# Performance work log

Hardware: AMD Instinct MI355X
Metric: run time of the kernel (lower is better)

The kernel has to match this reference:

```python
import jax, jax.numpy as jnp
import numpy as np

N_NODES = 50000
N_EDGES = 800000
N_GRAPHS = 64
D = 96              # input_dim = hidden_dim = output_dim
N_GIN = 4           # num_layers - 1 GINConv layers
N_HEADS = 5         # num_layers linear_prediction heads
BN_EPS = 1e-5


def setup_inputs() -> dict:
    key = jax.random.key(0)
    ks = jax.random.split(key, 16)
    s = 1.0 / np.sqrt(D)
    h = jax.random.normal(ks[0], (N_NODES, D), dtype=jnp.float32)
    src = jax.random.randint(ks[1], (N_EDGES,), 0, N_NODES, dtype=jnp.int32)
    dst = jax.random.randint(ks[2], (N_EDGES,), 0, N_NODES, dtype=jnp.int32)
    # sorted node->graph ids; deterministic so every graph is non-empty
    graph_ids = (jnp.arange(N_NODES, dtype=jnp.int32) * N_GRAPHS) // N_NODES
    return {
        "h": h,
        # GIN layer MLPs (num_mlp_layers=2): Linear -> BN -> ReLU -> Linear
        "gin_W1": jax.random.uniform(ks[3], (N_GIN, D, D), jnp.float32, -s, s),
        "gin_b1": jax.random.uniform(ks[4], (N_GIN, D), jnp.float32, -s, s),
        "gin_bn1_g": jnp.ones((N_GIN, D), jnp.float32),
        "gin_bn1_b": jnp.zeros((N_GIN, D), jnp.float32),
        "gin_W2": jax.random.uniform(ks[5], (N_GIN, D, D), jnp.float32, -s, s),
        "gin_b2": jax.random.uniform(ks[6], (N_GIN, D), jnp.float32, -s, s),
        # per-layer outer BatchNorm1d
        "bn_g": jnp.ones((N_GIN, D), jnp.float32),
        "bn_b": jnp.zeros((N_GIN, D), jnp.float32),
        # shared PReLU parameter (nn.PReLU default: 1 param, init 0.25)
        "prelu_a": jnp.full((1,), 0.25, jnp.float32),
        # linear_prediction heads
        "lin_W": jax.random.uniform(ks[7], (N_HEADS, D, D), jnp.float32, -s, s),
        "lin_b": jax.random.uniform(ks[8], (N_HEADS, D), jnp.float32, -s, s),
        "src": src,
        "dst": dst,
        "graph_ids": graph_ids,
    }


def _batchnorm(x, gamma, beta):
    # training-mode batch statistics over the node dim (biased variance, as torch)
    m = jnp.mean(x, axis=0)
    v = jnp.var(x, axis=0)
    return gamma * (x - m) * jax.lax.rsqrt(v + BN_EPS) + beta


def reference(h, gin_W1, gin_b1, gin_bn1_g, gin_bn1_b, gin_W2, gin_b2,
              bn_g, bn_b, prelu_a, lin_W, lin_b, src, dst, graph_ids):
    hidden_rep = [h]
    for l in range(N_GIN):
        # GINConv, sum aggregation, eps=0 (learn_eps=False): (1+eps)*h + sum_{j in N(i)} h_j
        agg = jax.ops.segment_sum(h[src], dst, num_segments=N_NODES)  # [N, D]
        z = h + agg
        # apply_func MLP: Linear -> BN -> ReLU -> Linear
        z = jax.nn.relu(_batchnorm(z @ gin_W1[l] + gin_b1[l], gin_bn1_g[l], gin_bn1_b[l]))
        z = z @ gin_W2[l] + gin_b2[l]
        # outer BatchNorm + PReLU
        z = _batchnorm(z, bn_g[l], bn_b[l])
        h = jnp.where(z >= 0, z, prelu_a * z)
        hidden_rep.append(h)
    # max graph pooling + per-layer linear heads (dropout = identity in eval)
    reps = []
    for l, hr in enumerate(hidden_rep):
        pooled = jax.ops.segment_max(hr, graph_ids, num_segments=N_GRAPHS)  # [B, D]
        reps.append(pooled @ lin_W[l] + lin_b[l])
    # layer_aggregation='cat': stack on dim=-1 then flatten -> [B, D * (N_GIN+1)]
    return jnp.stack(reps, axis=-1).reshape(N_GRAPHS, -1)
```

## Files before the change

kernel.cpp:

```cpp
#include <hip/hip_runtime.h>
#include <hip/hip_bf16.h>

#define N_NODES 50000
#define N_EDGES 800000
#define N_GRAPHS 64
#define D 96
#define N_GIN 4
#define BN_EPS 1e-5f
#define PCH 64
#define GEMM_GRID 782
#define LP 104
#define ELLCAP 64
#define SENT 50000

#define P1_BLOCKS 256
#define EPB 3125
#define BSH 8
#define BNODES 256
#define NBUCK 196
#define SPITCH 33

typedef __bf16 bf16;
typedef __bf16 bf16x8 __attribute__((ext_vector_type(8)));
typedef float f32x4 __attribute__((ext_vector_type(4)));
typedef unsigned short u16;
typedef unsigned int u32;
typedef unsigned short u16x8 __attribute__((ext_vector_type(8)));

__device__ inline unsigned enc(float f) {
    unsigned b = __float_as_uint(f);
    return (b & 0x80000000u) ? ~b : (b | 0x80000000u);
}
__device__ inline float dec(unsigned u) {
    return __uint_as_float((u & 0x80000000u) ? (u ^ 0x80000000u) : ~u);
}

__global__ void k_prolog(const float* __restrict__ h, bf16* __restrict__ hb,
                         bf16* __restrict__ hb1,
                         const float* __restrict__ W1, const float* __restrict__ W2,
                         bf16* __restrict__ wf, float* __restrict__ stats,
                         unsigned* __restrict__ pooledu) {
    int b = blockIdx.x;
    int tid = threadIdx.x;
    if (b < 2344) {
        int e = (b * 256 + tid) * 8;
        if (e >= N_NODES * D) return;
        float4 v0 = *(const float4*)(h + e);
        float4 v1 = *(const float4*)(h + e + 4);
        bf16x8 o;
        o[0] = (bf16)v0.x; o[1] = (bf16)v0.y; o[2] = (bf16)v0.z; o[3] = (bf16)v0.w;
        o[4] = (bf16)v1.x; o[5] = (bf16)v1.y; o[6] = (bf16)v1.z; o[7] = (bf16)v1.w;
        *(bf16x8*)(hb + e) = o;
    } else if (b < 2352) {
        int mat = b - 2344;
        const float* src = (mat < 4) ? (W1 + mat * D * D) : (W2 + (mat - 4) * D * D);
        bf16* dst = wf + mat * D * D;
        for (int p = tid; p < D * D; p += 256) {
            int f = p >> 9;
            int r = p & 511;
            int lane = r >> 3;
            int j = r & 7;
            int q = lane >> 4;
            int m16 = lane & 15;
            int nt = f / 3, ks = f % 3;
            int k = ks * 32 + q * 8 + j;
            int n = nt * 16 + m16;
            dst[p] = (bf16)src[k * D + n];
        }
    } else {
        int t = (b - 2352) * 256 + tid;
        if (t < N_GIN * 2 * 2 * D) stats[t] = 0.0f;
        if (t < 5 * N_GRAPHS * D) pooledu[t] = 0u;
        if (t < D) {
            hb[(size_t)SENT * D + t] = (bf16)0.0f;
            hb1[(size_t)SENT * D + t] = (bf16)0.0f;
        }
    }
}

__global__ void __launch_bounds__(256) k_part_pool(
        const int* __restrict__ src, const int* __restrict__ dst,
        u32* __restrict__ eo, u16* __restrict__ offs,
        const bf16* __restrict__ hb, unsigned* __restrict__ pooledu) {
    __shared__ u16 sdst[EPB + 3];
    __shared__ u16 ssrc[EPB + 3];
    __shared__ int hist[256];
    __shared__ int incl[256];
    int tid = threadIdx.x;
    if (blockIdx.x < P1_BLOCKS) {
        int e0 = blockIdx.x * EPB;
        hist[tid] = 0;
        __syncthreads();
        for (int i = tid; i < EPB; i += 256) {
            int d = dst[e0 + i];
            sdst[i] = (u16)d;
            ssrc[i] = (u16)src[e0 + i];
            atomicAdd(&hist[d >> BSH], 1);
        }
        __syncthreads();
        int v = hist[tid];
        incl[tid] = v;
        __syncthreads();
        for (int o = 1; o < 256; o <<= 1) {
            int t = (tid >= o) ? incl[tid - o] : 0;
            __syncthreads();
            incl[tid] += t;
            __syncthreads();
        }
        int ex = incl[tid] - v;
        if (tid <= NBUCK) offs[tid * P1_BLOCKS + blockIdx.x] = (u16)ex;
        hist[tid] = ex;
        __syncthreads();
        for (int i = tid; i < EPB; i += 256) {
            int d = sdst[i];
            int pos = atomicAdd(&hist[d >> BSH], 1);
            eo[e0 + pos] = ((u32)(d & (BNODES - 1)) << 16) | (u32)ssrc[i];
        }
    } else {
        int grp = (blockIdx.x - P1_BLOCKS) * 16 + (tid >> 4);
        int l = tid & 15;
        if (l >= 12) return;
        int g = grp / PCH, c = grp % PCH;
        int gs = (g * N_NODES + N_GRAPHS - 1) / N_GRAPHS;
        int ge = ((g + 1) * N_NODES + N_GRAPHS - 1) / N_GRAPHS;
        int len = ge - gs;
        int rs = gs + (len * c) / PCH;
        int re = gs + (len * (c + 1)) / PCH;
        const bf16x8* __restrict__ base = (const bf16x8*)hb;
        float m[8];
#pragma unroll
        for (int j = 0; j < 8; ++j) m[j] = -3e38f;
        int i = rs;
        for (; i + 2 <= re; i += 2) {
            bf16x8 r0 = base[i * 12 + l];
            bf16x8 r1 = base[(i + 1) * 12 + l];
#pragma unroll
            for (int j = 0; j < 8; ++j) m[j] = fmaxf(m[j], fmaxf((float)r0[j], (float)r1[j]));
        }
        if (i < re) {
            bf16x8 r = base[i * 12 + l];
#pragma unroll
            for (int j = 0; j < 8; ++j) m[j] = fmaxf(m[j], (float)r[j]);
        }
        unsigned* dstp = pooledu + (size_t)g * D + l * 8;
#pragma unroll
        for (int j = 0; j < 8; ++j) atomicMax(&dstp[j], enc(m[j]));
    }
}

__global__ void __launch_bounds__(256) k_ell_build(
        const u32* __restrict__ eo, const u16* __restrict__ offs,
        u16* __restrict__ ell, int* __restrict__ cnt) {
    __shared__ u32 sell32[BNODES * SPITCH];
    __shared__ int scnt[BNODES];
    int tid = threadIdx.x;
    int b = blockIdx.x;
    for (int i = tid; i < BNODES * SPITCH; i += 256) sell32[i] = 0xC350C350u;
    scnt[tid] = 0;
    __syncthreads();
    int beg = offs[b * P1_BLOCKS + tid];
    int end = offs[(b + 1) * P1_BLOCKS + tid];
    const u32* ep = eo + (size_t)tid * EPB;
    u16* srows = (u16*)sell32;
    for (int i = beg; i < end; ++i) {
        u32 pk = ep[i];
        int dl = pk >> 16;
        int pos = atomicAdd(&scnt[dl], 1);
        if (pos < ELLCAP) srows[dl * (2 * SPITCH) + pos] = (u16)pk;
    }
    __syncthreads();
    int node0 = b << BSH;
    int nn = min(BNODES, N_NODES - node0);
    if (tid < nn) cnt[node0 + tid] = scnt[tid];
    u32* gell = (u32*)(ell + (size_t)node0 * ELLCAP);
    for (int i = tid; i < nn * 32; i += 256) {
        gell[i] = sell32[(i >> 5) * SPITCH + (i & 31)];
    }
}

__global__ void __launch_bounds__(256) k_agg_gemm(
        const bf16* __restrict__ prev, const int* __restrict__ cnt,
        const u16* __restrict__ ell, const bf16* __restrict__ Bf,
        const float* __restrict__ bias, bf16* __restrict__ Z,
        float* __restrict__ ssum, float* __restrict__ sssq) {
    __shared__ bf16 sA[4][16 * LP];
    __shared__ float sr1[4][D], sr2[4][D];
    int tid = threadIdx.x;
    int lane = tid & 63, wv = tid >> 6;
    int q = lane >> 4, m16 = lane & 15;
    int strip = blockIdx.x * 4 + wv;

    float psum[6], pssq[6];
#pragma unroll
    for (int f = 0; f < 6; ++f) { psum[f] = 0.0f; pssq[f] = 0.0f; }

    if (strip < 3125) {
        const bf16x8* __restrict__ base = (const bf16x8*)prev;
        int gl = m16;
        if (gl < 12) {
#pragma unroll 1
            for (int rp = 0; rp < 2; ++rp) {
                int nA = strip * 16 + rp * 8 + q;
                int nB = nA + 4;
                float accA[8], accB[8];
                bf16x8 selfA = base[nA * 12 + gl];
                bf16x8 selfB = base[nB * 12 + gl];
#pragma unroll
                for (int j = 0; j < 8; ++j) { accA[j] = (float)selfA[j]; accB[j] = (float)selfB[j]; }
                int dgA = cnt[nA]; if (dgA > ELLCAP) dgA = ELLCAP;
                int dgB = cnt[nB]; if (dgB > ELLCAP) dgB = ELLCAP;
                int dgr = (((dgA > dgB) ? dgA : dgB) + 7) & ~7;
                const u16* epA = ell + (size_t)nA * ELLCAP;
                const u16* epB = ell + (size_t)nB * ELLCAP;
                for (int e = 0; e < dgr; e += 8) {
                    u16x8 ivA = *(const u16x8*)(epA + e);
                    u16x8 ivB = *(const u16x8*)(epB + e);
                    bf16x8 a0 = base[(int)ivA[0] * 12 + gl];
                    bf16x8 a1 = base[(int)ivA[1] * 12 + gl];
                    bf16x8 a2 = base[(int)ivA[2] * 12 + gl];
                    bf16x8 a3 = base[(int)ivA[3] * 12 + gl];
                    bf16x8 a4 = base[(int)ivA[4] * 12 + gl];
                    bf16x8 a5 = base[(int)ivA[5] * 12 + gl];
                    bf16x8 a6 = base[(int)ivA[6] * 12 + gl];
                    bf16x8 a7 = base[(int)ivA[7] * 12 + gl];
                    bf16x8 b0 = base[(int)ivB[0] * 12 + gl];
                    bf16x8 b1 = base[(int)ivB[1] * 12 + gl];
                    bf16x8 b2 = base[(int)ivB[2] * 12 + gl];
                    bf16x8 b3 = base[(int)ivB[3] * 12 + gl];
                    bf16x8 b4 = base[(int)ivB[4] * 12 + gl];
                    bf16x8 b5 = base[(int)ivB[5] * 12 + gl];
                    bf16x8 b6 = base[(int)ivB[6] * 12 + gl];
                    bf16x8 b7 = base[(int)ivB[7] * 12 + gl];
#pragma unroll
                    for (int j = 0; j < 8; ++j) {
                        accA[j] += (float)a0[j] + (float)a1[j] + (float)a2[j] + (float)a3[j]
                                 + (float)a4[j] + (float)a5[j] + (float)a6[j] + (float)a7[j];
                        accB[j] += (float)b0[j] + (float)b1[j] + (float)b2[j] + (float)b3[j]
                                 + (float)b4[j] + (float)b5[j] + (float)b6[j] + (float)b7[j];
                    }
                }
                bf16x8 oA, oB;
#pragma unroll
                for (int j = 0; j < 8; ++j) { oA[j] = (bf16)accA[j]; oB[j] = (bf16)accB[j]; }
                *(bf16x8*)&sA[wv][(rp * 8 + q) * LP + gl * 8] = oA;
                *(bf16x8*)&sA[wv][(rp * 8 + 4 + q) * LP + gl * 8] = oB;
            }
        }
        __asm__ volatile("s_waitcnt lgkmcnt(0)" ::: "memory");

        bf16x8 bfr[18];
#pragma unroll
        for (int f = 0; f < 18; ++f) bfr[f] = *(const bf16x8*)(Bf + (f * 64 + lane) * 8);

        bf16x8 a0 = *(const bf16x8*)&sA[wv][m16 * LP + q * 8];
        bf16x8 a1 = *(const bf16x8*)&sA[wv][m16 * LP + 32 + q * 8];
        bf16x8 a2 = *(const bf16x8*)&sA[wv][m16 * LP + 64 + q * 8];

#pragma unroll
        for (int f = 0; f < 6; ++f) {
            f32x4 acc = {0.0f, 0.0f, 0.0f, 0.0f};
            acc = __builtin_amdgcn_mfma_f32_16x16x32_bf16(a0, bfr[f * 3 + 0], acc, 0, 0, 0);
            acc = __builtin_amdgcn_mfma_f32_16x16x32_bf16(a1, bfr[f * 3 + 1], acc, 0, 0, 0);
            acc = __builtin_amdgcn_mfma_f32_16x16x32_bf16(a2, bfr[f * 3 + 2], acc, 0, 0, 0);
            int col = f * 16 + m16;
            float bvf = bias[col];
            bf16* zp = Z + (size_t)(strip * 16 + q * 4) * D + col;
#pragma unroll
            for (int i = 0; i < 4; ++i) {
                float v = acc[i] + bvf;
                zp[(size_t)i * D] = (bf16)v;
                psum[f] += v;
                pssq[f] += v * v;
            }
        }
    }
#pragma unroll
    for (int f = 0; f < 6; ++f) {
        float r = psum[f];
        r += __shfl_xor(r, 16);
        r += __shfl_xor(r, 32);
        float r2 = pssq[f];
        r2 += __shfl_xor(r2, 16);
        r2 += __shfl_xor(r2, 32);
        if (lane < 16) {
            sr1[wv][f * 16 + lane] = r;
            sr2[wv][f * 16 + lane] = r2;
        }
    }
    __syncthreads();
    int t = wv * 64 + lane;
    if (t < D) {
        atomicAdd(&ssum[t], sr1[0][t] + sr1[1][t] + sr1[2][t] + sr1[3][t]);
    } else if (t < 2 * D) {
        int u = t - D;
        atomicAdd(&sssq[u], sr2[0][u] + sr2[1][u] + sr2[2][u] + sr2[3][u]);
    }
}

__global__ void k_transform(const bf16* __restrict__ Z, const float* __restrict__ st,
                            const float* __restrict__ gamma, const float* __restrict__ beta,
                            const float* __restrict__ pa, bf16* __restrict__ O) {
    __shared__ float cs[D], ct[D];
    int t = threadIdx.x;
    if (t < D) {
        float m = st[t] * (1.0f / N_NODES);
        float v = st[D + t] * (1.0f / N_NODES) - m * m;
        float inv = rsqrtf(v + BN_EPS);
        float sc = gamma[t] * inv;
        cs[t] = sc;
        ct[t] = beta[t] - m * sc;
    }
    __syncthreads();
    int e = (blockIdx.x * 256 + t) * 8;
    if (e >= N_NODES * D) return;
    float alpha = pa[0];
    int c = e % D;
    bf16x8 z = *(const bf16x8*)(Z + e);
    bf16x8 o;
#pragma unroll
    for (int j = 0; j < 8; ++j) {
        float v = (float)z[j] * cs[c + j] + ct[c + j];
        o[j] = (bf16)(v >= 0.0f ? v : alpha * v);
    }
    *(bf16x8*)(O + e) = o;
}

__global__ void __launch_bounds__(256) k_gemm_fused(
        const bf16* __restrict__ A, const bf16* __restrict__ Bf,
        const float* __restrict__ st, const float* __restrict__ gamma,
        const float* __restrict__ beta, const float* __restrict__ bias,
        bf16* __restrict__ Z, float* __restrict__ ssum, float* __restrict__ sssq,
        unsigned* __restrict__ poolu) {
    __shared__ float cs[D], ct[D];
    __shared__ float sr1[4][D];
    __shared__ float sr2[4][D];
    __shared__ unsigned pmax[2 * D];
    int tid = threadIdx.x;
    if (tid < D) {
        float m = st[tid] * (1.0f / N_NODES);
        float v = st[D + tid] * (1.0f / N_NODES) - m * m;
        float inv = rsqrtf(v + BN_EPS);
        float sc = gamma[tid] * inv;
        cs[tid] = sc;
        ct[tid] = beta[tid] - m * sc;
    }
    if (tid < 2 * D) pmax[tid] = 0u;
    __syncthreads();

    int lane = tid & 63;
    int wv = tid >> 6;
    int w = (blockIdx.x * blockDim.x + tid) >> 6;
    int nw = (gridDim.x * blockDim.x) >> 6;
    int q = lane >> 4, m16 = lane & 15;
    int g0 = (int)(((long long)blockIdx.x * 64) * N_GRAPHS / N_NODES);

    float as_[3][8], at_[3][8];
#pragma unroll
    for (int ks = 0; ks < 3; ++ks)
#pragma unroll
        for (int j = 0; j < 8; ++j) {
            as_[ks][j] = cs[ks * 32 + q * 8 + j];
            at_[ks][j] = ct[ks * 32 + q * 8 + j];
        }

    bf16x8 bfr[18];
#pragma unroll
    for (int f = 0; f < 18; ++f) bfr[f] = *(const bf16x8*)(Bf + (f * 64 + lane) * 8);
    float bv[6];
#pragma unroll
    for (int f = 0; f < 6; ++f) bv[f] = bias[f * 16 + m16];
    float psum[6], pssq[6];
#pragma unroll
    for (int f = 0; f < 6; ++f) { psum[f] = 0.0f; pssq[f] = 0.0f; }

    const int NSTRIP = N_NODES / 16;
    for (int s = w; s < NSTRIP; s += nw) {
        const bf16* arow = A + (size_t)(s * 16 + m16) * D;
        bf16x8 z0 = *(const bf16x8*)(arow + q * 8);
        bf16x8 z1 = *(const bf16x8*)(arow + 32 + q * 8);
        bf16x8 z2 = *(const bf16x8*)(arow + 64 + q * 8);
        bf16x8 a0, a1, a2;
#pragma unroll
        for (int j = 0; j < 8; ++j) {
            a0[j] = (bf16)fmaxf(0.0f, (float)z0[j] * as_[0][j] + at_[0][j]);
            a1[j] = (bf16)fmaxf(0.0f, (float)z1[j] * as_[1][j] + at_[1][j]);
            a2[j] = (bf16)fmaxf(0.0f, (float)z2[j] * as_[2][j] + at_[2][j]);
        }
#pragma unroll
        for (int f = 0; f < 6; ++f) {
            f32x4 acc = {0.0f, 0.0f, 0.0f, 0.0f};
            acc = __builtin_amdgcn_mfma_f32_16x16x32_bf16(a0, bfr[f * 3 + 0], acc, 0, 0, 0);
            acc = __builtin_amdgcn_mfma_f32_16x16x32_bf16(a1, bfr[f * 3 + 1], acc, 0, 0, 0);
            acc = __builtin_amdgcn_mfma_f32_16x16x32_bf16(a2, bfr[f * 3 + 2], acc, 0, 0, 0);
            int col = f * 16 + m16;
            bf16* zp = Z + (size_t)(s * 16 + q * 4) * D + col;
#pragma unroll
            for (int i = 0; i < 4; ++i) {
                float v = acc[i] + bv[f];
                zp[(size_t)i * D] = (bf16)v;
                psum[f] += v;
                pssq[f] += v * v;
                int row = s * 16 + q * 4 + i;
                int g = (int)(((unsigned)row * 64u) / 50000u);
                int slot = g - g0;
                if (slot >= 0 && slot < 2)
                    atomicMax(&pmax[slot * D + col], enc(v));
            }
        }
    }
#pragma unroll
    for (int f = 0; f < 6; ++f) {
        float r = psum[f];
        r += __shfl_xor(r, 16);
        r += __shfl_xor(r, 32);
        float r2 = pssq[f];
        r2 += __shfl_xor(r2, 16);
        r2 += __shfl_xor(r2, 32);
        if (lane < 16) {
            sr1[wv][f * 16 + lane] = r;
            sr2[wv][f * 16 + lane] = r2;
        }
    }
    __syncthreads();
    int t = wv * 64 + lane;
    if (t < D) {
        atomicAdd(&ssum[t], sr1[0][t] + sr1[1][t] + sr1[2][t] + sr1[3][t]);
    } else if (t < 2 * D) {
        int u = t - D;
        atomicAdd(&sssq[u], sr2[0][u] + sr2[1][u] + sr2[2][u] + sr2[3][u]);
    }
    if (t < 2 * D) {
        int sl = t / D, c = t % D;
        int gg = g0 + sl;
        if (gg < N_GRAPHS && pmax[t] != 0u)
            atomicMax(&poolu[gg * D + c], pmax[t]);
    }
}

__global__ void k_heads(const unsigned* __restrict__ pooledu, const float* __restrict__ stats,
                        const float* __restrict__ bng, const float* __restrict__ bnb,
                        const float* __restrict__ pa, const float* __restrict__ W,
                        const float* __restrict__ B, float* __restrict__ out) {
    __shared__ float pv[D];
    int b = blockIdx.x;
    int l = b >> 6;
    int g = b & 63;
    int d = threadIdx.x;
    if (d < D) {
        float m = dec(pooledu[(size_t)(l * N_GRAPHS + g) * D + d]);
        if (l > 0) {
            int gl = l - 1;
            const float* st = stats + (gl * 2 + 1) * 2 * D;
            float mean = st[d] * (1.0f / N_NODES);
            float var = st[D + d] * (1.0f / N_NODES) - mean * mean;
            float inv = rsqrtf(var + BN_EPS);
            float s = bng[gl * D + d] * inv;
            float t = bnb[gl * D + d] - mean * s;
            float v = m * s + t;
            m = (v >= 0.0f) ? v : pa[0] * v;
        }
        pv[d] = m;
    }
    __syncthreads();
    if (d >= D) return;
    const float* w = W + (size_t)l * D * D;
    float acc = B[l * D + d];
    for (int k = 0; k < D; ++k) acc += pv[k] * w[k * D + d];
    out[g * (5 * D) + d * 5 + l] = acc;
}

extern "C" void kernel_launch(void* const* d_in, const int* in_sizes, int n_in,
                              void* d_out, int out_size, void* d_ws, size_t ws_size,
                              hipStream_t stream) {
    const float* h     = (const float*)d_in[0];
    const float* gW1   = (const float*)d_in[1];
    const float* gb1   = (const float*)d_in[2];
    const float* bn1g  = (const float*)d_in[3];
    const float* bn1b  = (const float*)d_in[4];
    const float* gW2   = (const float*)d_in[5];
    const float* gb2   = (const float*)d_in[6];
    const float* bng   = (const float*)d_in[7];
    const float* bnb   = (const float*)d_in[8];
    const float* prelu = (const float*)d_in[9];
    const float* linW  = (const float*)d_in[10];
    const float* linb  = (const float*)d_in[11];
    const int*   srcv  = (const int*)d_in[12];
    const int*   dstv  = (const int*)d_in[13];
    float* out = (float*)d_out;

    char* base = (char*)d_ws;
    size_t off = 0;
    auto carve = [&](size_t bytes) -> void* {
        void* p = base + off;
        off += (bytes + 255) & ~(size_t)255;
        return p;
    };
    const size_t HB = (size_t)N_NODES * D;
    bf16* hb0   = (bf16*)carve((HB + D) * 2);
    bf16* hb1   = (bf16*)carve((HB + D) * 2);
    bf16* zb    = (bf16*)carve(HB * 2);
    bf16* ab    = (bf16*)carve(HB * 2);
    bf16* wf    = (bf16*)carve(8 * D * D * 2);
    float* stats = (float*)carve(N_GIN * 2 * 2 * D * 4);
    int* cnt    = (int*)carve((size_t)N_NODES * 4);
    u16* ell    = (u16*)carve((size_t)N_NODES * ELLCAP * 2);
    u32* eo     = (u32*)carve((size_t)N_EDGES * 4);
    u16* offs   = (u16*)carve((size_t)(NBUCK + 1) * P1_BLOCKS * 2);
    unsigned* pooledu = (unsigned*)carve(5 * N_GRAPHS * D * 4);

    k_prolog<<<2472, 256, 0, stream>>>(h, hb0, hb1, gW1, gW2, wf, stats, pooledu);
    k_part_pool<<<P1_BLOCKS + N_GRAPHS * PCH / 16, 256, 0, stream>>>(
        srcv, dstv, eo, offs, hb0, pooledu);
    k_ell_build<<<NBUCK, 256, 0, stream>>>(eo, offs, ell, cnt);

    const bf16* prev = hb0;
    for (int l = 0; l < N_GIN; ++l) {
        float* st1 = stats + (l * 2 + 0) * 2 * D;
        float* st2 = stats + (l * 2 + 1) * 2 * D;
        if (l > 0) {
            float* stp = stats + ((l - 1) * 2 + 1) * 2 * D;
            k_transform<<<2344, 256, 0, stream>>>(ab, stp, bng + (l - 1) * D,
                                                  bnb + (l - 1) * D, prelu, hb1);
            prev = hb1;
        }
        k_agg_gemm<<<GEMM_GRID, 256, 0, stream>>>(prev, cnt, ell, wf + l * D * D,
                                                  gb1 + l * D, zb, st1, st1 + D);
        k_gemm_fused<<<GEMM_GRID, 256, 0, stream>>>(zb, wf + (4 + l) * D * D, st1,
                                                    bn1g + l * D, bn1b + l * D,
                                                    gb2 + l * D, ab, st2, st2 + D,
                                                    pooledu + (size_t)(l + 1) * N_GRAPHS * D);
    }
    k_heads<<<5 * N_GRAPHS, 128, 0, stream>>>(pooledu, stats, bng, bnb, prelu,
                                              linW, linb, out);
}
```

Measured before the change: 429.6 us.

## Pipeline neighbor gathers through an LDS ring via async global_load_lds

Rewrites the aggregation phase of the fused agg+GEMM kernel. The strip's ELL indices are first staged into LDS, then neighbor rows are streamed through a per-wave ring buffer of async global->LDS loads with a fixed prefetch depth. The aim is to keep several gathers in flight per wave and hide gather latency, replacing the earlier unrolled register loads done two rows at a time. In exchange it adds serial per-edge bookkeeping, processes only one edge per iteration, uses more LDS (which may lower occupancy), and relies on sentinel rows and vmcnt waits being correct.

```diff
diff --git a/kernel.cpp b/kernel.cpp
--- a/kernel.cpp
+++ b/kernel.cpp
@@ -12,6 +12,7 @@
 #define LP 104
 #define ELLCAP 64
 #define SENT 50000
+#define RING_K 6
 
 #define P1_BLOCKS 256
 #define EPB 3125
@@ -25,7 +26,14 @@
 typedef float f32x4 __attribute__((ext_vector_type(4)));
 typedef unsigned short u16;
 typedef unsigned int u32;
-typedef unsigned short u16x8 __attribute__((ext_vector_type(8)));
+
+#define WAITVM(N) asm volatile("s_waitcnt vmcnt(" #N ")" ::: "memory")
+
+__device__ __forceinline__ void gload16(const void* g, void* l) {
+    __builtin_amdgcn_global_load_lds(
+        (const __attribute__((address_space(1))) unsigned int*)g,
+        (__attribute__((address_space(3))) unsigned int*)l, 16, 0, 0);
+}
 
 __device__ inline unsigned enc(float f) {
     unsigned b = __float_as_uint(f);
@@ -183,11 +191,13 @@
         const u16* __restrict__ ell, const bf16* __restrict__ Bf,
         const float* __restrict__ bias, bf16* __restrict__ Z,
         float* __restrict__ ssum, float* __restrict__ sssq) {
+    __shared__ __align__(16) char ring[4][RING_K * 1024];
+    __shared__ __align__(16) u16 sIdx[4][1024];
     __shared__ bf16 sA[4][16 * LP];
     __shared__ float sr1[4][D], sr2[4][D];
     int tid = threadIdx.x;
     int lane = tid & 63, wv = tid >> 6;
-    int q = lane >> 4, m16 = lane & 15;
+    int g = lane >> 4, m16 = lane & 15;
     int strip = blockIdx.x * 4 + wv;
 
     float psum[6], pssq[6];
@@ -195,59 +205,122 @@
     for (int f = 0; f < 6; ++f) { psum[f] = 0.0f; pssq[f] = 0.0f; }
 
     if (strip < 3125) {
-        const bf16x8* __restrict__ base = (const bf16x8*)prev;
-        int gl = m16;
-        if (gl < 12) {
+        const char* hbase = (const char*)prev;
+        char* ringW = (char*)&ring[wv][0];
+        u16* sIdxW = &sIdx[wv][0];
+        int c16 = (m16 < 12) ? m16 * 16 : 0;
+
+        gload16((const char*)ell + (size_t)strip * 2048 + lane * 16, (char*)sIdxW);
+        gload16((const char*)ell + (size_t)strip * 2048 + 1024 + lane * 16,
+                (char*)sIdxW + 1024);
+        const bf16x8* base8 = (const bf16x8*)prev;
+        bf16x8 self0 = base8[(strip * 16 + 0 + g) * 12 + m16];
+        bf16x8 self1 = base8[(strip * 16 + 4 + g) * 12 + m16];
+        bf16x8 self2 = base8[(strip * 16 + 8 + g) * 12 + m16];
+        bf16x8 self3 = base8[(strip * 16 + 12 + g) * 12 + m16];
+        int degv = cnt[strip * 16 + m16];
+        if (degv > ELLCAP) degv = ELLCAP;
+        WAITVM(0);
+        int dg0 = max(max(__shfl(degv, 0), __shfl(degv, 1)),
+                      max(__shfl(degv, 2), __shfl(degv, 3)));
+        int dg1 = max(max(__shfl(degv, 4), __shfl(degv, 5)),
+                      max(__shfl(degv, 6), __shfl(degv, 7)));
+        int dg2 = max(max(__shfl(degv, 8), __shfl(degv, 9)),
+                      max(__shfl(degv, 10), __shfl(degv, 11)));
+        int dg3 = max(max(__shfl(degv, 12), __shfl(degv, 13)),
+                      max(__shfl(degv, 14), __shfl(degv, 15)));
+        dg0 = (dg0 + 7) & ~7;
+        dg1 = (dg1 + 7) & ~7;
+        dg2 = (dg2 + 7) & ~7;
+        dg3 = (dg3 + 7) & ~7;
+        int total = dg0 + dg1 + dg2 + dg3;
+
+        if (m16 < 12) {
+            if (dg0 == 0) *(bf16x8*)&sA[wv][(0 + g) * LP + m16 * 8] = self0;
+            if (dg1 == 0) *(bf16x8*)&sA[wv][(4 + g) * LP + m16 * 8] = self1;
+            if (dg2 == 0) *(bf16x8*)&sA[wv][(8 + g) * LP + m16 * 8] = self2;
+            if (dg3 == 0) *(bf16x8*)&sA[wv][(12 + g) * LP + m16 * 8] = self3;
+        }
+
+        int ri = 0, si = 0;
+        while (ri < 4 && ((ri == 0) ? dg0 : (ri == 1) ? dg1 : (ri == 2) ? dg2 : dg3) == 0) ri++;
 #pragma unroll 1
-            for (int rp = 0; rp < 2; ++rp) {
-                int nA = strip * 16 + rp * 8 + q;
-                int nB = nA + 4;
-                float accA[8], accB[8];
-                bf16x8 selfA = base[nA * 12 + gl];
-                bf16x8 selfB = base[nB * 12 + gl];
-#pragma unroll
-                for (int j = 0; j < 8; ++j) { accA[j] = (float)selfA[j]; accB[j] = (float)selfB[j]; }
-                int dgA = cnt[nA]; if (dgA > ELLCAP) dgA = ELLCAP;
-                int dgB = cnt[nB]; if (dgB > ELLCAP) dgB = ELLCAP;
-                int dgr = (((dgA > dgB) ? dgA : dgB) + 7) & ~7;
-                const u16* epA = ell + (size_t)nA * ELLCAP;
-                const u16* epB = ell + (size_t)nB * ELLCAP;
-                for (int e = 0; e < dgr; e += 8) {
-                    u16x8 ivA = *(const u16x8*)(epA + e);
-                    u16x8 ivB = *(const u16x8*)(epB + e);
-                    bf16x8 a0 = base[(int)ivA[0] * 12 + gl];
-                    bf16x8 a1 = base[(int)ivA[1] * 12 + gl];
-                    bf16x8 a2 = base[(int)ivA[2] * 12 + gl];
-                    bf16x8 a3 = base[(int)ivA[3] * 12 + gl];
-                    bf16x8 a4 = base[(int)ivA[4] * 12 + gl];
-                    bf16x8 a5 = base[(int)ivA[5] * 12 + gl];
-                    bf16x8 a6 = base[(int)ivA[6] * 12 + gl];
-                    bf16x8 a7 = base[(int)ivA[7] * 12 + gl];
-                    bf16x8 b0 = base[(int)ivB[0] * 12 + gl];
-                    bf16x8 b1 = base[(int)ivB[1] * 12 + gl];
-                    bf16x8 b2 = base[(int)ivB[2] * 12 + gl];
-                    bf16x8 b3 = base[(int)ivB[3] * 12 + gl];
-                    bf16x8 b4 = base[(int)ivB[4] * 12 + gl];
-                    bf16x8 b5 = base[(int)ivB[5] * 12 + gl];
-                    bf16x8 b6 = base[(int)ivB[6] * 12 + gl];
-                    bf16x8 b7 = base[(int)ivB[7] * 12 + gl];
-#pragma unroll
-                    for (int j = 0; j < 8; ++j) {
-                        accA[j] += (float)a0[j] + (float)a1[j] + (float)a2[j] + (float)a3[j]
-                                 + (float)a4[j] + (float)a5[j] + (float)a6[j] + (float)a7[j];
-                        accB[j] += (float)b0[j] + (float)b1[j] + (float)b2[j] + (float)b3[j]
-                                 + (float)b4[j] + (float)b5[j] + (float)b6[j] + (float)b7[j];
-                    }
+        for (int p = 0; p < RING_K - 1; ++p) {
+            int idx;
+            if (ri < 4) {
+                idx = sIdxW[(ri * 4 + g) * 64 + si];
+                si++;
+                int dcur = (ri == 0) ? dg0 : (ri == 1) ? dg1 : (ri == 2) ? dg2 : dg3;
+                if (si >= dcur) {
+                    si = 0; ri++;
+                    while (ri < 4 && ((ri == 0) ? dg0 : (ri == 1) ? dg1 : (ri == 2) ? dg2 : dg3) == 0) ri++;
                 }
-                bf16x8 oA, oB;
-#pragma unroll
-                for (int j = 0; j < 8; ++j) { oA[j] = (bf16)accA[j]; oB[j] = (bf16)accB[j]; }
-                *(bf16x8*)&sA[wv][(rp * 8 + q) * LP + gl * 8] = oA;
-                *(bf16x8*)&sA[wv][(rp * 8 + 4 + q) * LP + gl * 8] = oB;
+            } else idx = SENT;
+            gload16(hbase + (size_t)idx * 192 + c16, ringW + p * 1024);
+        }
+        int nidx;
+        if (ri < 4) {
+            nidx = sIdxW[(ri * 4 + g) * 64 + si];
+            si++;
+            int dcur = (ri == 0) ? dg0 : (ri == 1) ? dg1 : (ri == 2) ? dg2 : dg3;
+            if (si >= dcur) {
+                si = 0; ri++;
+                while (ri < 4 && ((ri == 0) ? dg0 : (ri == 1) ? dg1 : (ri == 2) ? dg2 : dg3) == 0) ri++;
             }
-        }
+        } else nidx = SENT;
+
+        int rc = 0;
+        while (rc < 4 && ((rc == 0) ? dg0 : (rc == 1) ? dg1 : (rc == 2) ? dg2 : dg3) == 0) rc++;
+        int sc = 0;
+        int dcons = (rc == 0) ? dg0 : (rc == 1) ? dg1 : (rc == 2) ? dg2 : dg3;
+        float acc[8];
+        {
+            bf16x8 s0 = (rc == 0) ? self0 : (rc == 1) ? self1 : (rc == 2) ? self2 : self3;
+#pragma unroll
+            for (int j = 0; j < 8; ++j) acc[j] = (float)s0[j];
+        }
+        int slot_c = 0;
+        int slot_i = RING_K - 1;
+
+#pragma unroll 1
+        for (int t = 0; t < total; ++t) {
+            WAITVM(4);
+            bf16x8 v = *(const bf16x8*)(ringW + slot_c * 1024 + lane * 16);
+            gload16(hbase + (size_t)nidx * 192 + c16, ringW + slot_i * 1024);
+            if (ri < 4) {
+                nidx = sIdxW[(ri * 4 + g) * 64 + si];
+                si++;
+                int dcur = (ri == 0) ? dg0 : (ri == 1) ? dg1 : (ri == 2) ? dg2 : dg3;
+                if (si >= dcur) {
+                    si = 0; ri++;
+                    while (ri < 4 && ((ri == 0) ? dg0 : (ri == 1) ? dg1 : (ri == 2) ? dg2 : dg3) == 0) ri++;
+                }
+            } else nidx = SENT;
+#pragma unroll
+            for (int j = 0; j < 8; ++j) acc[j] += (float)v[j];
+            sc++;
+            if (sc >= dcons) {
+                bf16x8 o;
+#pragma unroll
+                for (int j = 0; j < 8; ++j) o[j] = (bf16)acc[j];
+                if (m16 < 12) *(bf16x8*)&sA[wv][(rc * 4 + g) * LP + m16 * 8] = o;
+                rc++;
+                while (rc < 4 && ((rc == 0) ? dg0 : (rc == 1) ? dg1 : (rc == 2) ? dg2 : dg3) == 0) rc++;
+                sc = 0;
+                if (rc < 4) {
+                    dcons = (rc == 1) ? dg1 : (rc == 2) ? dg2 : dg3;
+                    bf16x8 sf = (rc == 1) ? self1 : (rc == 2) ? self2 : self3;
+#pragma unroll
+                    for (int j = 0; j < 8; ++j) acc[j] = (float)sf[j];
+                }
+            }
+            slot_c++; if (slot_c == RING_K) slot_c = 0;
+            slot_i++; if (slot_i == RING_K) slot_i = 0;
+        }
+
         __asm__ volatile("s_waitcnt lgkmcnt(0)" ::: "memory");
 
+        int q = g;
         bf16x8 bfr[18];
 #pragma unroll
         for (int f = 0; f < 18; ++f) bfr[f] = *(const bf16x8*)(Bf + (f * 64 + lane) * 8);
@@ -258,16 +331,16 @@
 
 #pragma unroll
         for (int f = 0; f < 6; ++f) {
-            f32x4 acc = {0.0f, 0.0f, 0.0f, 0.0f};
-            acc = __builtin_amdgcn_mfma_f32_16x16x32_bf16(a0, bfr[f * 3 + 0], acc, 0, 0, 0);
-            acc = __builtin_amdgcn_mfma_f32_16x16x32_bf16(a1, bfr[f * 3 + 1], acc, 0, 0, 0);
-            acc = __builtin_amdgcn_mfma_f32_16x16x32_bf16(a2, bfr[f * 3 + 2], acc, 0, 0, 0);
+            f32x4 acc2 = {0.0f, 0.0f, 0.0f, 0.0f};
+            acc2 = __builtin_amdgcn_mfma_f32_16x16x32_bf16(a0, bfr[f * 3 + 0], acc2, 0, 0, 0);
+            acc2 = __builtin_amdgcn_mfma_f32_16x16x32_bf16(a1, bfr[f * 3 + 1], acc2, 0, 0, 0);
+            acc2 = __builtin_amdgcn_mfma_f32_16x16x32_bf16(a2, bfr[f * 3 + 2], acc2, 0, 0, 0);
             int col = f * 16 + m16;
             float bvf = bias[col];
             bf16* zp = Z + (size_t)(strip * 16 + q * 4) * D + col;
 #pragma unroll
             for (int i = 0; i < 4; ++i) {
-                float v = acc[i] + bvf;
+                float v = acc2[i] + bvf;
                 zp[(size_t)i * D] = (bf16)v;
                 psum[f] += v;
                 pssq[f] += v * v;
```

Measured after the change: 588.5 us. 37.0% more time.

## Partition ELL neighbor lists into three source-node ranges for gather locality

Applied to the files above, without the earlier changes.

The ELL build now counts each destination's edges per source-index third, pads each segment to a multiple of eight, and stores them in range order with packed segment offsets in cnt. The aggregation kernel walks the three segments in sequence so that, across all waves, gathers concentrate on one third of the feature table at a time, aiming for better L2/MALL hit rates. In exchange it pays an extra counting pass over the edges, up to three rounds of padded sentinel gathers per node, and a larger ELL capacity of 72. Rows whose padded segments overflow 72 are truncated.

```diff
diff --git a/kernel.cpp b/kernel.cpp
--- a/kernel.cpp
+++ b/kernel.cpp
@@ -10,15 +10,17 @@
 #define PCH 64
 #define GEMM_GRID 782
 #define LP 104
-#define ELLCAP 64
+#define ELLCAP 72
 #define SENT 50000
+#define R1B 16667
+#define R2B 33334
 
 #define P1_BLOCKS 256
 #define EPB 3125
 #define BSH 8
 #define BNODES 256
 #define NBUCK 196
-#define SPITCH 33
+#define SPITCH 37
 
 typedef __bf16 bf16;
 typedef __bf16 bf16x8 __attribute__((ext_vector_type(8)));
@@ -152,29 +154,56 @@
         const u32* __restrict__ eo, const u16* __restrict__ offs,
         u16* __restrict__ ell, int* __restrict__ cnt) {
     __shared__ u32 sell32[BNODES * SPITCH];
-    __shared__ int scnt[BNODES];
+    __shared__ int sc[3][BNODES];
+    __shared__ int spk[BNODES];
     int tid = threadIdx.x;
     int b = blockIdx.x;
     for (int i = tid; i < BNODES * SPITCH; i += 256) sell32[i] = 0xC350C350u;
-    scnt[tid] = 0;
+    sc[0][tid] = 0; sc[1][tid] = 0; sc[2][tid] = 0;
     __syncthreads();
     int beg = offs[b * P1_BLOCKS + tid];
     int end = offs[(b + 1) * P1_BLOCKS + tid];
     const u32* ep = eo + (size_t)tid * EPB;
+    for (int i = beg; i < end; ++i) {
+        u32 pk = ep[i];
+        int dl = pk >> 16;
+        int s = (int)(pk & 0xFFFF);
+        int r = (s < R1B) ? 0 : ((s < R2B) ? 1 : 2);
+        atomicAdd(&sc[r][dl], 1);
+    }
+    __syncthreads();
+    {
+        int c0 = sc[0][tid], c1 = sc[1][tid], c2 = sc[2][tid];
+        int o1 = min((c0 + 7) & ~7, ELLCAP);
+        int o2 = min(o1 + ((c1 + 7) & ~7), ELLCAP);
+        int o3 = min(o2 + ((c2 + 7) & ~7), ELLCAP);
+        spk[tid] = o1 | (o2 << 8) | (o3 << 16);
+        sc[0][tid] = 0;
+        sc[1][tid] = o1;
+        sc[2][tid] = o2;
+    }
+    __syncthreads();
     u16* srows = (u16*)sell32;
     for (int i = beg; i < end; ++i) {
         u32 pk = ep[i];
         int dl = pk >> 16;
-        int pos = atomicAdd(&scnt[dl], 1);
-        if (pos < ELLCAP) srows[dl * (2 * SPITCH) + pos] = (u16)pk;
+        int s = (int)(pk & 0xFFFF);
+        int r = (s < R1B) ? 0 : ((s < R2B) ? 1 : 2);
+        int pos = atomicAdd(&sc[r][dl], 1);
+        int w = spk[dl];
+        int lim = (r == 0) ? (w & 255) : ((r == 1) ? ((w >> 8) & 255) : ((w >> 16) & 255));
+        if (pos < lim) srows[dl * (2 * SPITCH) + pos] = (u16)s;
     }
     __syncthreads();
     int node0 = b << BSH;
     int nn = min(BNODES, N_NODES - node0);
-    if (tid < nn) cnt[node0 + tid] = scnt[tid];
+    if (tid < nn) cnt[node0 + tid] = spk[tid];
     u32* gell = (u32*)(ell + (size_t)node0 * ELLCAP);
-    for (int i = tid; i < nn * 32; i += 256) {
-        gell[i] = sell32[(i >> 5) * SPITCH + (i & 31)];
+    const int ROWW = ELLCAP / 2;
+    for (int i = tid; i < nn * ROWW; i += 256) {
+        int row = i / ROWW;
+        int col = i - row * ROWW;
+        gell[i] = sell32[row * SPITCH + col];
     }
 }
 
@@ -198,6 +227,9 @@
         const bf16x8* __restrict__ base = (const bf16x8*)prev;
         int gl = m16;
         if (gl < 12) {
+            u16x8 sentv;
+#pragma unroll
+            for (int j = 0; j < 8; ++j) sentv[j] = (u16)SENT;
 #pragma unroll 1
             for (int rp = 0; rp < 2; ++rp) {
                 int nA = strip * 16 + rp * 8 + q;
@@ -207,36 +239,47 @@
                 bf16x8 selfB = base[nB * 12 + gl];
 #pragma unroll
                 for (int j = 0; j < 8; ++j) { accA[j] = (float)selfA[j]; accB[j] = (float)selfB[j]; }
-                int dgA = cnt[nA]; if (dgA > ELLCAP) dgA = ELLCAP;
-                int dgB = cnt[nB]; if (dgB > ELLCAP) dgB = ELLCAP;
-                int dgr = (((dgA > dgB) ? dgA : dgB) + 7) & ~7;
-                const u16* epA = ell + (size_t)nA * ELLCAP;
-                const u16* epB = ell + (size_t)nB * ELLCAP;
-                for (int e = 0; e < dgr; e += 8) {
-                    u16x8 ivA = *(const u16x8*)(epA + e);
-                    u16x8 ivB = *(const u16x8*)(epB + e);
-                    bf16x8 a0 = base[(int)ivA[0] * 12 + gl];
-                    bf16x8 a1 = base[(int)ivA[1] * 12 + gl];
-                    bf16x8 a2 = base[(int)ivA[2] * 12 + gl];
-                    bf16x8 a3 = base[(int)ivA[3] * 12 + gl];
-                    bf16x8 a4 = base[(int)ivA[4] * 12 + gl];
-                    bf16x8 a5 = base[(int)ivA[5] * 12 + gl];
-                    bf16x8 a6 = base[(int)ivA[6] * 12 + gl];
-                    bf16x8 a7 = base[(int)ivA[7] * 12 + gl];
-                    bf16x8 b0 = base[(int)ivB[0] * 12 + gl];
-                    bf16x8 b1 = base[(int)ivB[1] * 12 + gl];
-                    bf16x8 b2 = base[(int)ivB[2] * 12 + gl];
-                    bf16x8 b3 = base[(int)ivB[3] * 12 + gl];
-                    bf16x8 b4 = base[(int)ivB[4] * 12 + gl];
-                    bf16x8 b5 = base[(int)ivB[5] * 12 + gl];
-                    bf16x8 b6 = base[(int)ivB[6] * 12 + gl];
-                    bf16x8 b7 = base[(int)ivB[7] * 12 + gl];
-#pragma unroll
-                    for (int j = 0; j < 8; ++j) {
-                        accA[j] += (float)a0[j] + (float)a1[j] + (float)a2[j] + (float)a3[j]
-                                 + (float)a4[j] + (float)a5[j] + (float)a6[j] + (float)a7[j];
-                        accB[j] += (float)b0[j] + (float)b1[j] + (float)b2[j] + (float)b3[j]
-                                 + (float)b4[j] + (float)b5[j] + (float)b6[j] + (float)b7[j];
+                int wA = cnt[nA];
+                int wB = cnt[nB];
+                const u16* rowA = ell + (size_t)nA * ELLCAP;
+                const u16* rowB = ell + (size_t)nB * ELLCAP;
+#pragma unroll 1
+                for (int r = 0; r < 3; ++r) {
+                    int sA_ = (r == 0) ? 0 : ((r == 1) ? (wA & 255) : ((wA >> 8) & 255));
+                    int eA_ = (r == 0) ? (wA & 255) : ((r == 1) ? ((wA >> 8) & 255) : ((wA >> 16) & 255));
+                    int sB_ = (r == 0) ? 0 : ((r == 1) ? (wB & 255) : ((wB >> 8) & 255));
+                    int eB_ = (r == 0) ? (wB & 255) : ((r == 1) ? ((wB >> 8) & 255) : ((wB >> 16) & 255));
+                    int LA = eA_ - sA_, LB = eB_ - sB_;
+                    int dgr = (LA > LB) ? LA : LB;
+                    const u16* epA = rowA + sA_;
+                    const u16* epB = rowB + sB_;
+                    for (int e = 0; e < dgr; e += 8) {
+                        u16x8 ivA = sentv, ivB = sentv;
+                        if (e < LA) ivA = *(const u16x8*)(epA + e);
+                        if (e < LB) ivB = *(const u16x8*)(epB + e);
+                        bf16x8 a0 = base[(int)ivA[0] * 12 + gl];
+                        bf16x8 a1 = base[(int)ivA[1] * 12 + gl];
+                        bf16x8 a2 = base[(int)ivA[2] * 12 + gl];
+                        bf16x8 a3 = base[(int)ivA[3] * 12 + gl];
+                        bf16x8 a4 = base[(int)ivA[4] * 12 + gl];
+                        bf16x8 a5 = base[(int)ivA[5] * 12 + gl];
+                        bf16x8 a6 = base[(int)ivA[6] * 12 + gl];
+                        bf16x8 a7 = base[(int)ivA[7] * 12 + gl];
+                        bf16x8 b0 = base[(int)ivB[0] * 12 + gl];
+                        bf16x8 b1 = base[(int)ivB[1] * 12 + gl];
+                        bf16x8 b2 = base[(int)ivB[2] * 12 + gl];
+                        bf16x8 b3 = base[(int)ivB[3] * 12 + gl];
+                        bf16x8 b4 = base[(int)ivB[4] * 12 + gl];
+                        bf16x8 b5 = base[(int)ivB[5] * 12 + gl];
+                        bf16x8 b6 = base[(int)ivB[6] * 12 + gl];
+                        bf16x8 b7 = base[(int)ivB[7] * 12 + gl];
+#pragma unroll
+                        for (int j = 0; j < 8; ++j) {
+                            accA[j] += (float)a0[j] + (float)a1[j] + (float)a2[j] + (float)a3[j]
+                                     + (float)a4[j] + (float)a5[j] + (float)a6[j] + (float)a7[j];
+                            accB[j] += (float)b0[j] + (float)b1[j] + (float)b2[j] + (float)b3[j]
+                                     + (float)b4[j] + (float)b5[j] + (float)b6[j] + (float)b7[j];
+                        }
                     }
                 }
                 bf16x8 oA, oB;
```

Result: slower. 446.7 us (+4.0%).
